# Kernel optimization log

Measured on AMD Instinct MI355X. Metric: run time of the kernel, lower is better.

## Reference

```python
import jax, jax.numpy as jnp
import numpy as np

ALPHA = 0.25
GAMMA = 2.0
DELTA = 0.5
# class_weights dict {0:1, 1:4, 2:3, 3:2} as a lookup table
CLASS_WEIGHT_LUT = np.array([1.0, 4.0, 3.0, 2.0], dtype=np.float32)


def setup_inputs() -> dict:
    key = jax.random.key(0)
    k1, k2 = jax.random.split(key)
    B, N = 8, 4194304
    y_pred = jax.random.normal(k1, (B, N), dtype=jnp.float32) + 1.5
    # true break durations/classes in [0, 3)
    y_true = jax.random.uniform(k2, (B, N), dtype=jnp.float32, minval=0.0, maxval=3.0)
    return {"y_pred": y_pred, "y_true": y_true}


def reference(y_pred, y_true):
    p = y_pred.astype(jnp.float32).reshape(-1)
    t = y_true.astype(jnp.float32).reshape(-1)
    lut = jnp.asarray(CLASS_WEIGHT_LUT)
    # per-element class-weight lookup (vectorized gather)
    cls = jnp.clip(jnp.round(t), 0.0, 3.0).astype(jnp.int32)
    weights = lut[cls]
    d = jnp.abs(p - t)
    # focal weighting on normalized difficulty
    focal_w = jnp.clip(d / DELTA, 0.0, 1.0) ** GAMMA
    # smooth L1 (huber) with beta=DELTA, reduction='none'
    base = jnp.where(d < DELTA, 0.5 * d * d / DELTA, d - 0.5 * DELTA)
    return jnp.mean(ALPHA * focal_w * base * weights)
```

## Files before the change

kernel.cpp:

```cpp
#include <hip/hip_runtime.h>
#include <hip/hip_bf16.h>

#define ALPHA 0.25f
#define DELTA 0.5f

__global__ void __launch_bounds__(256)
dafl_partial_kernel(const float* __restrict__ y_pred,
                    const float* __restrict__ y_true,
                    float* __restrict__ partials,
                    long long n4)
{
    const float4* __restrict__ p4 = reinterpret_cast<const float4*>(y_pred);
    const float4* __restrict__ t4 = reinterpret_cast<const float4*>(y_true);

    float acc = 0.0f;
    long long idx = (long long)blockIdx.x * blockDim.x + threadIdx.x;
    long long stride = (long long)gridDim.x * blockDim.x;

    for (long long i = idx; i < n4; i += stride) {
        float4 p = p4[i];
        float4 t = t4[i];

        #pragma unroll
        for (int j = 0; j < 4; ++j) {
            float pp = (&p.x)[j];
            float tt = (&t.x)[j];

            float r = rintf(tt);
            r = fminf(fmaxf(r, 0.0f), 3.0f);
            int cls = (int)r;
            float w = (cls == 0) ? 1.0f
                    : (cls == 1) ? 4.0f
                    : (cls == 2) ? 3.0f
                    :              2.0f;

            float d = fabsf(pp - tt);
            float f = fminf(d * 2.0f, 1.0f);
            f = f * f;
            float base = (d < DELTA) ? (d * d) : (d - 0.25f);

            acc += ALPHA * f * base * w;
        }
    }

    #pragma unroll
    for (int off = 32; off > 0; off >>= 1)
        acc += __shfl_down(acc, off, 64);

    __shared__ float smem[4];
    int lane = threadIdx.x & 63;
    int wave = threadIdx.x >> 6;
    if (lane == 0) smem[wave] = acc;
    __syncthreads();

    if (threadIdx.x == 0) {
        float s = smem[0] + smem[1] + smem[2] + smem[3];
        partials[blockIdx.x] = s;
    }
}

__global__ void __launch_bounds__(256)
dafl_final_kernel(const float* __restrict__ partials,
                  float* __restrict__ out,
                  int num_partials,
                  float inv_n)
{
    float acc = 0.0f;
    for (int i = threadIdx.x; i < num_partials; i += 256)
        acc += partials[i];

    #pragma unroll
    for (int off = 32; off > 0; off >>= 1)
        acc += __shfl_down(acc, off, 64);

    __shared__ float smem[4];
    int lane = threadIdx.x & 63;
    int wave = threadIdx.x >> 6;
    if (lane == 0) smem[wave] = acc;
    __syncthreads();

    if (threadIdx.x == 0) {
        float s = smem[0] + smem[1] + smem[2] + smem[3];
        out[0] = s * inv_n;
    }
}

extern "C" void kernel_launch(void* const* d_in, const int* in_sizes, int n_in,
                              void* d_out, int out_size, void* d_ws, size_t ws_size,
                              hipStream_t stream) {
    const float* y_pred = (const float*)d_in[0];
    const float* y_true = (const float*)d_in[1];
    float* out = (float*)d_out;
    float* partials = (float*)d_ws;

    long long n = (long long)in_sizes[0];
    long long n4 = n >> 2;

    const int BLOCK = 256;
    const int GRID  = 2048;

    dafl_partial_kernel<<<GRID, BLOCK, 0, stream>>>(y_pred, y_true, partials, n4);
    dafl_final_kernel<<<1, BLOCK, 0, stream>>>(partials, out, GRID,
                                               1.0f / (double)n);
}
```

Before: 50.41 us.

## Fuse final reduction via last-block atomic counter and unroll main loop

Merges the two-kernel reduction into one kernel: each block publishes its partial, bumps an atomic counter, and the last block to finish sums all partials and writes the mean. The main loop now runs a fixed trip count with 32-bit indexing and unroll 4, with a separate tail loop, so more loads can be in flight. This removes the second kernel launch but adds a hipMemsetAsync per call and an atomic with fences at the end of every block.

```diff
diff --git a/kernel.cpp b/kernel.cpp
--- a/kernel.cpp
+++ b/kernel.cpp
@@ -3,24 +3,32 @@
 
 #define ALPHA 0.25f
 #define DELTA 0.5f
+#define GRID  2048
+#define BLOCK 256
 
-__global__ void __launch_bounds__(256)
-dafl_partial_kernel(const float* __restrict__ y_pred,
-                    const float* __restrict__ y_true,
-                    float* __restrict__ partials,
-                    long long n4)
+__global__ void __launch_bounds__(BLOCK)
+dafl_fused_kernel(const float* __restrict__ y_pred,
+                  const float* __restrict__ y_true,
+                  float* __restrict__ partials,
+                  unsigned int* __restrict__ counter,
+                  float* __restrict__ out,
+                  int n4,
+                  float inv_n)
 {
     const float4* __restrict__ p4 = reinterpret_cast<const float4*>(y_pred);
     const float4* __restrict__ t4 = reinterpret_cast<const float4*>(y_true);
 
+    const int idx    = blockIdx.x * BLOCK + threadIdx.x;
+    const int stride = GRID * BLOCK;
+    const int iters  = n4 / stride;
+
     float acc = 0.0f;
-    long long idx = (long long)blockIdx.x * blockDim.x + threadIdx.x;
-    long long stride = (long long)gridDim.x * blockDim.x;
+    int i = idx;
 
-    for (long long i = idx; i < n4; i += stride) {
+    #pragma unroll 4
+    for (int it = 0; it < iters; ++it, i += stride) {
         float4 p = p4[i];
         float4 t = t4[i];
-
         #pragma unroll
         for (int j = 0; j < 4; ++j) {
             float pp = (&p.x)[j];
@@ -42,46 +50,59 @@
             acc += ALPHA * f * base * w;
         }
     }
+    for (; i < n4; i += stride) {
+        float4 p = p4[i];
+        float4 t = t4[i];
+        #pragma unroll
+        for (int j = 0; j < 4; ++j) {
+            float pp = (&p.x)[j], tt = (&t.x)[j];
+            float r = rintf(tt);
+            r = fminf(fmaxf(r, 0.0f), 3.0f);
+            int cls = (int)r;
+            float w = (cls == 0) ? 1.0f : (cls == 1) ? 4.0f : (cls == 2) ? 3.0f : 2.0f;
+            float d = fabsf(pp - tt);
+            float f = fminf(d * 2.0f, 1.0f); f = f * f;
+            float base = (d < DELTA) ? (d * d) : (d - 0.25f);
+            acc += ALPHA * f * base * w;
+        }
+    }
 
     #pragma unroll
     for (int off = 32; off > 0; off >>= 1)
         acc += __shfl_down(acc, off, 64);
 
     __shared__ float smem[4];
-    int lane = threadIdx.x & 63;
-    int wave = threadIdx.x >> 6;
+    __shared__ int   s_done;
+    const int lane = threadIdx.x & 63;
+    const int wave = threadIdx.x >> 6;
     if (lane == 0) smem[wave] = acc;
     __syncthreads();
 
     if (threadIdx.x == 0) {
         float s = smem[0] + smem[1] + smem[2] + smem[3];
-        partials[blockIdx.x] = s;
+        __hip_atomic_store(&partials[blockIdx.x], s,
+                           __ATOMIC_RELAXED, __HIP_MEMORY_SCOPE_AGENT);
+        __threadfence();
+        unsigned int old = atomicAdd(counter, 1u);
+        s_done = (old == (GRID - 1u));
     }
-}
-
-__global__ void __launch_bounds__(256)
-dafl_final_kernel(const float* __restrict__ partials,
-                  float* __restrict__ out,
-                  int num_partials,
-                  float inv_n)
-{
-    float acc = 0.0f;
-    for (int i = threadIdx.x; i < num_partials; i += 256)
-        acc += partials[i];
-
-    #pragma unroll
-    for (int off = 32; off > 0; off >>= 1)
-        acc += __shfl_down(acc, off, 64);
-
-    __shared__ float smem[4];
-    int lane = threadIdx.x & 63;
-    int wave = threadIdx.x >> 6;
-    if (lane == 0) smem[wave] = acc;
     __syncthreads();
 
-    if (threadIdx.x == 0) {
-        float s = smem[0] + smem[1] + smem[2] + smem[3];
-        out[0] = s * inv_n;
+    if (s_done) {
+        float a2 = 0.0f;
+        for (int j = threadIdx.x; j < GRID; j += BLOCK)
+            a2 += __hip_atomic_load(&partials[j],
+                                    __ATOMIC_ACQUIRE, __HIP_MEMORY_SCOPE_AGENT);
+
+        #pragma unroll
+        for (int off = 32; off > 0; off >>= 1)
+            a2 += __shfl_down(a2, off, 64);
+
+        __syncthreads();
+        if (lane == 0) smem[wave] = a2;
+        __syncthreads();
+        if (threadIdx.x == 0)
+            out[0] = (smem[0] + smem[1] + smem[2] + smem[3]) * inv_n;
     }
 }
 
@@ -91,15 +112,15 @@
     const float* y_pred = (const float*)d_in[0];
     const float* y_true = (const float*)d_in[1];
     float* out = (float*)d_out;
-    float* partials = (float*)d_ws;
+
+    float* partials        = (float*)d_ws;
+    unsigned int* counter  = (unsigned int*)((char*)d_ws + GRID * sizeof(float));
 
     long long n = (long long)in_sizes[0];
-    long long n4 = n >> 2;
+    int n4 = (int)(n >> 2);
 
-    const int BLOCK = 256;
-    const int GRID  = 2048;
+    hipMemsetAsync(counter, 0, sizeof(unsigned int), stream);
 
-    dafl_partial_kernel<<<GRID, BLOCK, 0, stream>>>(y_pred, y_true, partials, n4);
-    dafl_final_kernel<<<1, BLOCK, 0, stream>>>(partials, out, GRID,
-                                               1.0f / (double)n);
+    dafl_fused_kernel<<<GRID, BLOCK, 0, stream>>>(
+        y_pred, y_true, partials, counter, out, n4, (float)(1.0 / (double)n));
 }
```

Measured after the change: 104.4 us. 2.07x slower.

## Fuse final reduction via packed fixed-point atomic with last-block completion

Applied to the files above, without the earlier changes.

Replaces the two-kernel partial/final reduction with a single kernel. Each block converts its sum to fixed point and atomically adds it to a 64-bit word whose low bits count finished blocks. The last block to arrive computes and writes the mean. This removes the second kernel launch and the partials round trip, at the cost of a memset before the launch, fixed-point rounding, and reliance on the packed sum not overflowing.

```diff
diff --git a/kernel.cpp b/kernel.cpp
--- a/kernel.cpp
+++ b/kernel.cpp
@@ -3,12 +3,20 @@
 
 #define ALPHA 0.25f
 #define DELTA 0.5f
+#define GRID  2048
+#define BLOCK 256
 
-__global__ void __launch_bounds__(256)
-dafl_partial_kernel(const float* __restrict__ y_pred,
-                    const float* __restrict__ y_true,
-                    float* __restrict__ partials,
-                    long long n4)
+#define CNT_BITS 12
+#define CNT_MASK 0xFFFull
+#define SCALE    1048576.0
+
+__global__ void __launch_bounds__(BLOCK)
+dafl_fused_kernel(const float* __restrict__ y_pred,
+                  const float* __restrict__ y_true,
+                  unsigned long long* __restrict__ acc_pack,
+                  float* __restrict__ out,
+                  long long n4,
+                  double inv_n_scaled)
 {
     const float4* __restrict__ p4 = reinterpret_cast<const float4*>(y_pred);
     const float4* __restrict__ t4 = reinterpret_cast<const float4*>(y_true);
@@ -48,40 +56,23 @@
         acc += __shfl_down(acc, off, 64);
 
     __shared__ float smem[4];
-    int lane = threadIdx.x & 63;
-    int wave = threadIdx.x >> 6;
+    const int lane = threadIdx.x & 63;
+    const int wave = threadIdx.x >> 6;
     if (lane == 0) smem[wave] = acc;
     __syncthreads();
 
     if (threadIdx.x == 0) {
         float s = smem[0] + smem[1] + smem[2] + smem[3];
-        partials[blockIdx.x] = s;
-    }
-}
 
-__global__ void __launch_bounds__(256)
-dafl_final_kernel(const float* __restrict__ partials,
-                  float* __restrict__ out,
-                  int num_partials,
-                  float inv_n)
-{
-    float acc = 0.0f;
-    for (int i = threadIdx.x; i < num_partials; i += 256)
-        acc += partials[i];
+        unsigned long long scaled =
+            (unsigned long long)((double)s * SCALE + 0.5);
+        unsigned long long old =
+            atomicAdd(acc_pack, (scaled << CNT_BITS) | 1ull);
 
-    #pragma unroll
-    for (int off = 32; off > 0; off >>= 1)
-        acc += __shfl_down(acc, off, 64);
-
-    __shared__ float smem[4];
-    int lane = threadIdx.x & 63;
-    int wave = threadIdx.x >> 6;
-    if (lane == 0) smem[wave] = acc;
-    __syncthreads();
-
-    if (threadIdx.x == 0) {
-        float s = smem[0] + smem[1] + smem[2] + smem[3];
-        out[0] = s * inv_n;
+        if ((old & CNT_MASK) == (unsigned long long)(GRID - 1)) {
+            unsigned long long total = (old >> CNT_BITS) + scaled;
+            out[0] = (float)((double)total * inv_n_scaled);
+        }
     }
 }
 
@@ -91,15 +82,14 @@
     const float* y_pred = (const float*)d_in[0];
     const float* y_true = (const float*)d_in[1];
     float* out = (float*)d_out;
-    float* partials = (float*)d_ws;
+    unsigned long long* acc_pack = (unsigned long long*)d_ws;
 
     long long n = (long long)in_sizes[0];
     long long n4 = n >> 2;
 
-    const int BLOCK = 256;
-    const int GRID  = 2048;
+    hipMemsetAsync(acc_pack, 0, sizeof(unsigned long long), stream);
 
-    dafl_partial_kernel<<<GRID, BLOCK, 0, stream>>>(y_pred, y_true, partials, n4);
-    dafl_final_kernel<<<1, BLOCK, 0, stream>>>(partials, out, GRID,
-                                               1.0f / (double)n);
+    dafl_fused_kernel<<<GRID, BLOCK, 0, stream>>>(
+        y_pred, y_true, acc_pack, out, n4,
+        1.0 / ((double)n * SCALE));
 }
```

Result: slower. 66.56 us (+32.0%).
